# Kernel optimization log

Measured on AMD Instinct MI355X. Metric: run time of the kernel, lower is better.

The kernel has to match this reference:

```python
import jax, jax.numpy as jnp
import numpy as np

BS, V, S, K = 4, 2048, 7, 10
CLASS_NUM, VEC_NUM, CAT = 6, 8, 16
OUT_HEAD = CLASS_NUM + VEC_NUM * 3  # 30
DIM_FUSE = 128 + 128 + 256 + 256 + 512 + 512 + 16  # 1808


def _normalize(x, axis):
    return x / jnp.maximum(jnp.linalg.norm(x, axis=axis, keepdims=True), 1e-12)


def knn_index(verts, k):
    # verts: (b, v, 3) -> (b, v, k) excluding self
    inner = jnp.einsum('bnd,bmd->bnm', verts, verts)
    sq = jnp.sum(verts * verts, axis=2)
    dist = sq[:, :, None] + sq[:, None, :] - 2.0 * inner
    _, idx = jax.lax.top_k(-dist, k + 1)
    return idx[:, :, 1:]


def nearest_index(target, source):
    # target: (b, v1, 3), source: (b, v2, 3) -> (b, v1)
    inner = jnp.einsum('bnd,bmd->bnm', target, source)
    d = jnp.sum(source * source, 2)[:, None, :] + jnp.sum(target * target, 2)[:, :, None] - 2.0 * inner
    return jnp.argmin(d, axis=-1)


def gather_nb(t, idx):
    # t: (b, v, d), idx: (b, v1, k) -> (b, v1, k, d)
    return jax.vmap(lambda tt, ii: tt[ii])(t, idx)


def gather1(t, idx):
    # t: (b, v, d), idx: (b, v1) -> (b, v1, d)
    return jax.vmap(lambda tt, ii: tt[ii])(t, idx)


def bn_train(x, g, b, eps=1e-5):
    # x: (b, v, c); BatchNorm1d training-mode over (batch, vertices)
    m = jnp.mean(x, axis=(0, 1), keepdims=True)
    v = jnp.var(x, axis=(0, 1), keepdims=True)
    return (x - m) * jax.lax.rsqrt(v + eps) * g + b


def conv_surface(nb_idx, verts, directions, s, kernel_num):
    nd = _normalize(gather_nb(verts, nb_idx) - verts[:, :, None, :], -1)  # (b,v,n,3)
    sd = _normalize(directions, 0)  # (3, s*k)
    theta = jax.nn.relu(jnp.einsum('bvnd,dk->bvnk', nd, sd))
    b_, v_, n_, _ = theta.shape
    theta = theta.reshape(b_, v_, n_, s, kernel_num)
    return jnp.sum(jnp.max(theta, axis=2), axis=2)  # (b, v, kernel_num)


def conv_layer(nb_idx, verts, fm, w, b, directions, s, out_ch):
    nd = _normalize(gather_nb(verts, nb_idx) - verts[:, :, None, :], -1)
    sd = _normalize(directions, 0)  # (3, s*out_ch)
    theta = jax.nn.relu(jnp.einsum('bvnd,dk->bvnk', nd, sd))  # (b,v,n,s*o)
    fo = jnp.einsum('bvc,ck->bvk', fm, w) + b  # (b, v, (s+1)*o)
    center = fo[..., :out_ch]
    supp = gather_nb(fo[..., out_ch:], nb_idx)  # (b,v,n,s*o)
    act = (theta * supp).reshape(theta.shape[0], theta.shape[1], theta.shape[2], s, out_ch)
    act = jnp.sum(jnp.max(act, axis=2), axis=2)  # (b, v, o)
    return center + act


def pool_layer(verts, fm, pooling_rate, nb_num):
    idx = knn_index(verts, nb_num)
    pooled = jnp.max(gather_nb(fm, idx), axis=2)
    pool_num = verts.shape[1] // pooling_rate
    # deterministic subsample (torch uses randperm; fixed arange for reproducibility)
    return verts[:, :pool_num], pooled[:, :pool_num]


def setup_inputs() -> dict:
    key = jax.random.key(0)
    ks = jax.random.split(key, 16)
    def rn(i, shape, scale=0.05):
        return jax.random.normal(ks[i], shape, dtype=jnp.float32) * scale
    z = lambda *s: jnp.zeros(s, jnp.float32)
    o = lambda *s: jnp.ones(s, jnp.float32)
    return {
        'vertices': jax.random.normal(ks[0], (BS, V, 3), dtype=jnp.float32),
        'onehot': jax.nn.one_hot(jax.random.randint(ks[1], (BS,), 0, CAT), CAT, dtype=jnp.float32),
        'dir0': rn(2, (3, S * 128)),
        'w1': rn(3, (128, (S + 1) * 128)), 'b1': z((S + 1) * 128), 'dir1': rn(4, (3, S * 128)),
        'w2': rn(5, (128, (S + 1) * 256)), 'b2': z((S + 1) * 256), 'dir2': rn(6, (3, S * 256)),
        'w3': rn(7, (256, (S + 1) * 256)), 'b3': z((S + 1) * 256), 'dir3': rn(8, (3, S * 256)),
        'w4': rn(9, (256, (S + 1) * 512)), 'b4': z((S + 1) * 512), 'dir4': rn(10, (3, S * 512)),
        'g_bn1': o(128), 'be_bn1': z(128),
        'g_bn2': o(256), 'be_bn2': z(256),
        'g_bn3': o(256), 'be_bn3': z(256),
        'wc1': rn(11, (512, DIM_FUSE)), 'bc1': z(512),
        'wc2': rn(12, (512, 512)), 'bc2': z(512),
        'wc3': rn(13, (OUT_HEAD, 512)), 'bc3': z(OUT_HEAD),
    }


def reference(vertices, onehot, dir0, w1, b1, dir1, w2, b2, dir2, w3, b3, dir3,
              w4, b4, dir4, g_bn1, be_bn1, g_bn2, be_bn2, g_bn3, be_bn3,
              wc1, bc1, wc2, bc2, wc3, bc3):
    bs, v_num, _ = vertices.shape
    nb = knn_index(vertices, K)
    fm0 = jax.nn.relu(conv_surface(nb, vertices, dir0, S, 128))
    fm1 = jax.nn.relu(bn_train(conv_layer(nb, vertices, fm0, w1, b1, dir1, S, 128), g_bn1, be_bn1))
    vp1, fp1 = pool_layer(vertices, fm1, 4, 4)
    nb1 = knn_index(vp1, min(K, vp1.shape[1] // 8))
    fm2 = jax.nn.relu(bn_train(conv_layer(nb1, vp1, fp1, w2, b2, dir2, S, 256), g_bn2, be_bn2))
    fm3 = jax.nn.relu(bn_train(conv_layer(nb1, vp1, fm2, w3, b3, dir3, S, 256), g_bn3, be_bn3))
    vp2, fp2 = pool_layer(vp1, fm3, 4, 4)
    nb2 = knn_index(vp2, min(K, vp2.shape[1] // 8))
    fm4 = conv_layer(nb2, vp2, fp2, w4, b4, dir4, S, 512)
    f_global = jnp.max(fm4, axis=1)  # (b, 512)
    n1 = nearest_index(vertices, vp1)
    n2 = nearest_index(vertices, vp2)
    fm2u = gather1(fm2, n1)
    fm3u = gather1(fm3, n1)
    fm4u = gather1(fm4, n2)
    fg = jnp.broadcast_to(f_global[:, None, :], (bs, v_num, 512))
    oh = jnp.broadcast_to(onehot[:, None, :], (bs, v_num, CAT))
    feat = jnp.concatenate([fm0, fm1, fm2u, fm3u, fm4u, oh], axis=2)
    fuse = jnp.concatenate([fm0, fm1, fm2u, fm3u, fm4u, fg, oh], axis=2)
    h = jax.nn.relu(jnp.einsum('bvc,oc->bvo', fuse, wc1) + bc1)
    h = jax.nn.relu(jnp.einsum('bvc,oc->bvo', h, wc2) + bc2)
    pred = jnp.einsum('bvc,oc->bvo', h, wc3) + bc3
    seg = pred[..., :CLASS_NUM]
    vecs = pred[..., CLASS_NUM:CLASS_NUM + VEC_NUM * 3]
    return (seg, vecs, feat)
```

## Files before the change

### kernel.cpp

```cpp
#include <hip/hip_runtime.h>
#include <hip/hip_bf16.h>
#include <math.h>

#define BSZ 4
#define VN 2048
#define SS 7
#define KNB 10

typedef __attribute__((ext_vector_type(8))) short short8;
typedef __attribute__((ext_vector_type(4))) float f32x4;

__device__ inline ushort f2bf(float x) {
    __hip_bfloat16 h = __float2bfloat16(x);
    return *(ushort*)&h;
}

__device__ inline unsigned fenc(float f) {
    unsigned b = __float_as_uint(f);
    return (b & 0x80000000u) ? ~b : (b | 0x80000000u);
}
__device__ inline float fdec(unsigned e) {
    unsigned b = (e & 0x80000000u) ? (e & 0x7FFFFFFFu) : ~e;
    return __uint_as_float(b);
}

#define PB0 8960L
#define PB1 24320L
#define PB2 958208L
#define PB3 1220352L
#define PB4 3186432L

__global__ void prep_uber(const float* __restrict__ d0, const float* __restrict__ d1,
                          const float* __restrict__ d2, const float* __restrict__ d3,
                          const float* __restrict__ d4,
                          float* __restrict__ s0, float* __restrict__ s1,
                          float* __restrict__ s2, float* __restrict__ s3, float* __restrict__ s4,
                          const float* __restrict__ wc3, float* __restrict__ wc3t,
                          const float* __restrict__ wc1, ushort* __restrict__ wc1b,
                          const float* __restrict__ wc2, ushort* __restrict__ wc2b,
                          const float* __restrict__ w1, const float* __restrict__ w2,
                          const float* __restrict__ w3, const float* __restrict__ w4,
                          ushort* __restrict__ o1, ushort* __restrict__ o2,
                          ushort* __restrict__ o3, ushort* __restrict__ o4) {
    long i = blockIdx.x * 256L + threadIdx.x;
    if (i < PB0) {
        const float* src; float* dst; int C, c;
        if (i < 896)        { src = d0; dst = s0; C = 896;  c = (int)i; }
        else if (i < 1792)  { src = d1; dst = s1; C = 896;  c = (int)i - 896; }
        else if (i < 3584)  { src = d2; dst = s2; C = 1792; c = (int)i - 1792; }
        else if (i < 5376)  { src = d3; dst = s3; C = 1792; c = (int)i - 3584; }
        else                { src = d4; dst = s4; C = 3584; c = (int)i - 5376; }
        float a = src[c], b = src[C + c], e = src[2 * C + c];
        float den = fmaxf(sqrtf(a * a + b * b + e * e), 1e-12f);
        dst[c] = a / den; dst[C + c] = b / den; dst[2 * C + c] = e / den;
    } else if (i < PB1) {
        long j = i - PB0;
        int o = (int)(j / 512), k = (int)(j % 512);
        wc3t[(long)k * 30 + o] = wc3[j];
    } else if (i < PB2) {
        long j = i - PB1;
        int c = (int)(j % 1824);
        long r = j / 1824;
        wc1b[j] = f2bf(c < 1808 ? wc1[r * 1808 + c] : 0.f);
    } else if (i < PB3) {
        long j = i - PB2;
        wc2b[j] = f2bf(wc2[j]);
    } else if (i < PB4) {
        long j = i - PB3;
        const float* w; ushort* o; int K, N;
        if (j < 131072)       { w = w1; o = o1; K = 128; N = 1024; }
        else if (j < 393216)  { w = w2; o = o2; K = 128; N = 2048; j -= 131072; }
        else if (j < 917504)  { w = w3; o = o3; K = 256; N = 2048; j -= 393216; }
        else                  { w = w4; o = o4; K = 256; N = 4096; j -= 917504; }
        int n = (int)(j / K), k = (int)(j % K);
        o[j] = f2bf(w[(long)k * N + n]);
    }
}

#define KOFF0 0L
#define KOFF1 1310720L
#define KOFF2 1392640L
#define KOFF3 1397760L
#define KOFF4 1528832L
#define KTOT  1537024L

template <int KK>
__device__ void knn_part_dev(const float* __restrict__ verts, int Nsrc, int T, int nch,
                             int tile, int b, int ch,
                             float* __restrict__ pd, int* __restrict__ pi,
                             float* sx, float* sy, float* sz) {
    int len = Nsrc / nch;
    const float* vb = verts + (long)b * VN * 3;
    int j0 = ch * len;
    for (int j = threadIdx.x; j < len; j += 256) {
        sx[j] = vb[(j0 + j) * 3 + 0];
        sy[j] = vb[(j0 + j) * 3 + 1];
        sz[j] = vb[(j0 + j) * 3 + 2];
    }
    __syncthreads();
    int i = tile * 256 + threadIdx.x;
    if (i >= T) return;
    float px = vb[i * 3], py = vb[i * 3 + 1], pz = vb[i * 3 + 2];
    float d[KK]; int id[KK];
#pragma unroll
    for (int q = 0; q < KK; q++) { d[q] = 1e30f; id[q] = 0; }
    for (int j = 0; j < len; j++) {
        float dx = sx[j] - px, dy = sy[j] - py, dz = sz[j] - pz;
        float dd = dx * dx + dy * dy + dz * dz;
        int jj = j0 + j;
        dd = (jj == i) ? 1e30f : dd;
        if (__any(dd < d[KK - 1])) {
#pragma unroll
            for (int q = 0; q < KK; q++) {
                bool lt = dd < d[q];
                float dmin = lt ? dd : d[q];
                float dmax = lt ? d[q] : dd;
                int imin = lt ? jj : id[q];
                int imax = lt ? id[q] : jj;
                d[q] = dmin; id[q] = imin; dd = dmax; jj = imax;
            }
        }
    }
    long base = (((long)b * T + i) * nch + ch) * KK;
#pragma unroll
    for (int q = 0; q < KK; q++) { pd[base + q] = d[q]; pi[base + q] = id[q]; }
}

__device__ void nearest_dev(const float* __restrict__ verts, int SN, int* __restrict__ out,
                            int gl, float* sx, float* sy, float* sz) {
    int t = gl * 256 + threadIdx.x;
    int b = t / VN;
    const float* vb = verts + (long)b * VN * 3;
    for (int j = threadIdx.x; j < SN; j += 256) {
        sx[j] = vb[j * 3]; sy[j] = vb[j * 3 + 1]; sz[j] = vb[j * 3 + 2];
    }
    __syncthreads();
    int i = t % VN;
    float px = vb[i * 3], py = vb[i * 3 + 1], pz = vb[i * 3 + 2];
    float best = 1e30f; int bi = 0;
    for (int j = 0; j < SN; j++) {
        float dx = sx[j] - px, dy = sy[j] - py, dz = sz[j] - pz;
        float dd = dx * dx + dy * dy + dz * dz;
        bool lt = dd < best;
        best = lt ? dd : best;
        bi = lt ? j : bi;
    }
    out[t] = bi;
}

__global__ __launch_bounds__(256) void knn_part_uber(const float* __restrict__ verts,
                                                     float* __restrict__ pd, int* __restrict__ pi,
                                                     int* __restrict__ n1, int* __restrict__ n2) {
    __shared__ float smem[3 * 512];
    int gb = blockIdx.x;
    if (gb < 512) {
        int tile = gb % 8, bc = gb / 8;
        knn_part_dev<10>(verts, 2048, 2048, 16, tile, bc / 16, bc % 16, pd + KOFF0, pi + KOFF0,
                         smem, smem + 128, smem + 256);
    } else if (gb < 544) {
        int local = gb - 512, tile = local % 2, bc = local / 2;
        knn_part_dev<10>(verts, 512, 512, 4, tile, bc / 4, bc % 4, pd + KOFF1, pi + KOFF1,
                         smem, smem + 128, smem + 256);
    } else if (gb < 548) {
        int bc = gb - 544;
        knn_part_dev<10>(verts, 128, 128, 1, 0, bc, 0, pd + KOFF2, pi + KOFF2,
                         smem, smem + 128, smem + 256);
    } else if (gb < 676) {
        int local = gb - 548, tile = local % 2, bc = local / 2;
        knn_part_dev<4>(verts, 2048, 512, 16, tile, bc / 16, bc % 16, pd + KOFF3, pi + KOFF3,
                        smem, smem + 128, smem + 256);
    } else if (gb < 692) {
        int bc = gb - 676;
        knn_part_dev<4>(verts, 512, 128, 4, 0, bc / 4, bc % 4, pd + KOFF4, pi + KOFF4,
                        smem, smem + 128, smem + 256);
    } else if (gb < 724) {
        nearest_dev(verts, 512, n1, gb - 692, smem, smem + 512, smem + 1024);
    } else {
        nearest_dev(verts, 128, n2, gb - 724, smem, smem + 512, smem + 1024);
    }
}

template <int KK, int NCH>
__device__ void knn_merge_dev(const float* __restrict__ pd, const int* __restrict__ pi,
                              int t, int* __restrict__ out) {
    float d[KK]; int id[KK];
#pragma unroll
    for (int q = 0; q < KK; q++) { d[q] = 1e30f; id[q] = 0; }
    for (int c = 0; c < NCH; c++) {
        long base = ((long)t * NCH + c) * KK;
        for (int q = 0; q < KK; q++) {
            float dd = pd[base + q];
            if (dd >= d[KK - 1]) break;
            int jj = pi[base + q];
#pragma unroll
            for (int p = 0; p < KK; p++) {
                bool lt = dd < d[p];
                float dmin = lt ? dd : d[p];
                float dmax = lt ? d[p] : dd;
                int imin = lt ? jj : id[p];
                int imax = lt ? id[p] : jj;
                d[p] = dmin; id[p] = imin; dd = dmax; jj = imax;
            }
        }
    }
#pragma unroll
    for (int q = 0; q < KK; q++) out[(long)t * KK + q] = id[q];
}

__global__ void knn_merge_uber(const float* __restrict__ pd, const int* __restrict__ pi,
                               int* __restrict__ nb, int* __restrict__ nb1, int* __restrict__ nb2,
                               int* __restrict__ nbp1, int* __restrict__ nbp2) {
    int gt = blockIdx.x * 256 + threadIdx.x;
    if (gt < 8192)       knn_merge_dev<10, 16>(pd + KOFF0, pi + KOFF0, gt, nb);
    else if (gt < 10240) knn_merge_dev<10, 4>(pd + KOFF1, pi + KOFF1, gt - 8192, nb1);
    else if (gt < 10752) knn_merge_dev<10, 1>(pd + KOFF2, pi + KOFF2, gt - 10240, nb2);
    else if (gt < 12800) knn_merge_dev<4, 16>(pd + KOFF3, pi + KOFF3, gt - 10752, nbp1);
    else                 knn_merge_dev<4, 4>(pd + KOFF4, pi + KOFF4, gt - 12800, nbp2);
}

__global__ void conv_surface_kernel(const float* __restrict__ verts, const int* __restrict__ nb,
                                    const float* __restrict__ sd, float* __restrict__ fm0,
                                    ushort* __restrict__ fm0b) {
    int bv = blockIdx.x;
    int b = bv / VN, v = bv % VN;
    __shared__ float snd[KNB][3];
    int tid = threadIdx.x;
    if (tid < KNB) {
        int nj = nb[(long)bv * KNB + tid];
        const float* vb = verts + (long)b * VN * 3;
        float dx = vb[nj * 3] - vb[v * 3];
        float dy = vb[nj * 3 + 1] - vb[v * 3 + 1];
        float dz = vb[nj * 3 + 2] - vb[v * 3 + 2];
        float den = fmaxf(sqrtf(dx * dx + dy * dy + dz * dz), 1e-12f);
        snd[tid][0] = dx / den; snd[tid][1] = dy / den; snd[tid][2] = dz / den;
    }
    __syncthreads();
    int c = tid;
    float acc = 0.f;
    for (int s = 0; s < SS; s++) {
        int col = s * 128 + c;
        float s0 = sd[col], s1 = sd[896 + col], s2 = sd[2 * 896 + col];
        float m = 0.f;
#pragma unroll
        for (int n = 0; n < KNB; n++) {
            float dot = snd[n][0] * s0 + snd[n][1] * s1 + snd[n][2] * s2;
            m = fmaxf(m, dot);
        }
        acc += m;
    }
    fm0[(long)bv * 128 + c] = acc;
    fm0b[(long)bv * 128 + c] = f2bf(acc);
}

__global__ void conv_act_kernel(const float* __restrict__ verts, const int* __restrict__ nb,
                                const float* __restrict__ sd, const float* __restrict__ fo,
                                float* __restrict__ out, unsigned* __restrict__ fgmax,
                                int Vl, int outC) {
    int bv = blockIdx.x;
    int b = bv / Vl, v = bv % Vl;
    __shared__ float snd[KNB][3];
    __shared__ int srow[KNB];
    int tid = threadIdx.x;
    if (tid < KNB) {
        int nj = nb[(long)bv * KNB + tid];
        srow[tid] = b * Vl + nj;
        const float* vb = verts + (long)b * VN * 3;
        float dx = vb[nj * 3] - vb[v * 3];
        float dy = vb[nj * 3 + 1] - vb[v * 3 + 1];
        float dz = vb[nj * 3 + 2] - vb[v * 3 + 2];
        float den = fmaxf(sqrtf(dx * dx + dy * dy + dz * dz), 1e-12f);
        snd[tid][0] = dx / den; snd[tid][1] = dy / den; snd[tid][2] = dz / den;
    }
    __syncthreads();
    int c = tid;
    int SC = SS * outC;
    int foN = SC + outC;
    float acc = fo[(long)bv * foN + c];
    for (int s = 0; s < SS; s++) {
        int col = s * outC + c;
        float s0 = sd[col], s1 = sd[SC + col], s2 = sd[2 * SC + col];
        float m = -1e30f;
#pragma unroll
        for (int n = 0; n < KNB; n++) {
            float dot = snd[n][0] * s0 + snd[n][1] * s1 + snd[n][2] * s2;
            float th = fmaxf(dot, 0.f);
            float sup = fo[(long)srow[n] * foN + outC + col];
            m = fmaxf(m, th * sup);
        }
        acc += m;
    }
    out[(long)bv * outC + c] = acc;
    if (fgmax) atomicMax(&fgmax[b * outC + c], fenc(acc));
}

__global__ __launch_bounds__(256) void bn_stat_kernel(const float* __restrict__ x,
                                                      float* __restrict__ stat, int R, int C) {
    int rp = 256 / C;
    int c = threadIdx.x % C;
    int rs = threadIdx.x / C;
    float s = 0.f, s2 = 0.f;
    for (long r = (long)blockIdx.x * rp + rs; r < R; r += (long)gridDim.x * rp) {
        float v = x[r * C + c];
        s += v; s2 += v * v;
    }
    atomicAdd(&stat[c], s);
    atomicAdd(&stat[C + c], s2);
}

__global__ void bn_apply_relu_kernel(const float* __restrict__ x, const float* __restrict__ stat,
                                     const float* __restrict__ g, const float* __restrict__ be,
                                     float* __restrict__ out, ushort* __restrict__ outb, int R, int C) {
    long i = blockIdx.x * 256L + threadIdx.x;
    if (i >= (long)R * C) return;
    int c = (int)(i % C);
    float mu = stat[c] / R;
    float var = stat[C + c] / R - mu * mu;
    var = fmaxf(var, 0.f);
    float y = (x[i] - mu) * rsqrtf(var + 1e-5f) * g[c] + be[c];
    y = fmaxf(y, 0.f);
    out[i] = y;
    if (outb) outb[i] = f2bf(y);
}

__global__ void pool_b_kernel(const float* __restrict__ fm, const int* __restrict__ idx,
                              ushort* __restrict__ out, int Vin, int T, int C) {
    long i = blockIdx.x * 256L + threadIdx.x;
    if (i >= (long)BSZ * T * C) return;
    int c = (int)(i % C);
    long bt = i / C;
    int b = (int)(bt / T), t = (int)(bt % T);
    const int* id = idx + ((long)b * T + t) * 4;
    float m = -1e30f;
#pragma unroll
    for (int n = 0; n < 4; n++)
        m = fmaxf(m, fm[((long)b * Vin + id[n]) * C + c]);
    out[i] = f2bf(m);
}

__global__ __launch_bounds__(256) void gemm_mfma_bt_kernel(
    const ushort* __restrict__ A, const ushort* __restrict__ Bt,
    const float* __restrict__ bias, float* __restrict__ Cf, ushort* __restrict__ Cb,
    int M, int N, int K, int relu)
{
    __shared__ ushort As[128 * 32];
    __shared__ ushort Bs[128 * 32];
    int t = threadIdx.x;
    int w = t >> 6, l = t & 63;
    int quad = l >> 4, lm = l & 15;
    int wm = w >> 1, wn = w & 1;
    long m0 = blockIdx.y * 128L;
    long n0 = blockIdx.x * 128L;
    int lr = t >> 2;
    int lk = (t & 3) * 8;
    f32x4 acc[4][4];
#pragma unroll
    for (int i = 0; i < 4; i++)
#pragma unroll
        for (int j = 0; j < 4; j++) acc[i][j] = (f32x4){0.f, 0.f, 0.f, 0.f};

    for (int k0 = 0; k0 < K; k0 += 32) {
        uint4 a0 = *(const uint4*)(A + (m0 + lr) * K + k0 + lk);
        uint4 a1 = *(const uint4*)(A + (m0 + 64 + lr) * K + k0 + lk);
        uint4 b0 = *(const uint4*)(Bt + (n0 + lr) * K + k0 + lk);
        uint4 b1 = *(const uint4*)(Bt + (n0 + 64 + lr) * K + k0 + lk);
        __syncthreads();
        *(uint4*)&As[lr * 32 + lk] = a0;
        *(uint4*)&As[(64 + lr) * 32 + lk] = a1;
        *(uint4*)&Bs[lr * 32 + lk] = b0;
        *(uint4*)&Bs[(64 + lr) * 32 + lk] = b1;
        __syncthreads();
        short8 af[4], bfr[4];
#pragma unroll
        for (int i = 0; i < 4; i++)
            af[i] = *(const short8*)&As[(wm * 64 + i * 16 + lm) * 32 + quad * 8];
#pragma unroll
        for (int j = 0; j < 4; j++)
            bfr[j] = *(const short8*)&Bs[(wn * 64 + j * 16 + lm) * 32 + quad * 8];
#pragma unroll
        for (int i = 0; i < 4; i++)
#pragma unroll
            for (int j = 0; j < 4; j++)
                acc[i][j] = __builtin_amdgcn_mfma_f32_16x16x32_bf16(af[i], bfr[j], acc[i][j], 0, 0, 0);
    }
#pragma unroll
    for (int i = 0; i < 4; i++) {
#pragma unroll
        for (int j = 0; j < 4; j++) {
            int n = (int)n0 + wn * 64 + j * 16 + lm;
            float bv = bias[n];
#pragma unroll
            for (int r = 0; r < 4; r++) {
                int m = (int)m0 + wm * 64 + i * 16 + quad * 4 + r;
                float v = acc[i][j][r] + bv;
                if (relu) v = fmaxf(v, 0.f);
                if (Cf) Cf[(long)m * N + n] = v;
                if (Cb) Cb[(long)m * N + n] = f2bf(v);
            }
        }
    }
}

__global__ __launch_bounds__(256) void gemm_mfma_bt64_kernel(
    const ushort* __restrict__ A, const ushort* __restrict__ Bt,
    const float* __restrict__ bias, float* __restrict__ Cf, ushort* __restrict__ Cb,
    int M, int N, int K, int relu)
{
    __shared__ ushort As[64 * 32];
    __shared__ ushort Bs[128 * 32];
    int t = threadIdx.x;
    int w = t >> 6, l = t & 63;
    int quad = l >> 4, lm = l & 15;
    int wm = w >> 1, wn = w & 1;
    long m0 = blockIdx.y * 64L;
    long n0 = blockIdx.x * 128L;
    int lr = t >> 2;
    int lk = (t & 3) * 8;
    f32x4 acc[2][4];
#pragma unroll
    for (int i = 0; i < 2; i++)
#pragma unroll
        for (int j = 0; j < 4; j++) acc[i][j] = (f32x4){0.f, 0.f, 0.f, 0.f};

    for (int k0 = 0; k0 < K; k0 += 32) {
        uint4 a0 = *(const uint4*)(A + (m0 + lr) * K + k0 + lk);
        uint4 b0 = *(const uint4*)(Bt + (n0 + lr) * K + k0 + lk);
        uint4 b1 = *(const uint4*)(Bt + (n0 + 64 + lr) * K + k0 + lk);
        __syncthreads();
        *(uint4*)&As[lr * 32 + lk] = a0;
        *(uint4*)&Bs[lr * 32 + lk] = b0;
        *(uint4*)&Bs[(64 + lr) * 32 + lk] = b1;
        __syncthreads();
        short8 af[2], bfr[4];
#pragma unroll
        for (int i = 0; i < 2; i++)
            af[i] = *(const short8*)&As[(wm * 32 + i * 16 + lm) * 32 + quad * 8];
#pragma unroll
        for (int j = 0; j < 4; j++)
            bfr[j] = *(const short8*)&Bs[(wn * 64 + j * 16 + lm) * 32 + quad * 8];
#pragma unroll
        for (int i = 0; i < 2; i++)
#pragma unroll
            for (int j = 0; j < 4; j++)
                acc[i][j] = __builtin_amdgcn_mfma_f32_16x16x32_bf16(af[i], bfr[j], acc[i][j], 0, 0, 0);
    }
#pragma unroll
    for (int i = 0; i < 2; i++) {
#pragma unroll
        for (int j = 0; j < 4; j++) {
            int n = (int)n0 + wn * 64 + j * 16 + lm;
            float bv = bias[n];
#pragma unroll
            for (int r = 0; r < 4; r++) {
                int m = (int)m0 + wm * 32 + i * 16 + quad * 4 + r;
                float v = acc[i][j][r] + bv;
                if (relu) v = fmaxf(v, 0.f);
                if (Cf) Cf[(long)m * N + n] = v;
                if (Cb) Cb[(long)m * N + n] = f2bf(v);
            }
        }
    }
}

__global__ __launch_bounds__(256) void wc3_kernel(const float* __restrict__ h2,
                                                  const float* __restrict__ wc3t,
                                                  const float* __restrict__ bc3,
                                                  float* __restrict__ out) {
    int r8 = threadIdx.x >> 5;
    int c = threadIdx.x & 31;
    long row = blockIdx.x * 8L + r8;
    const float* hr = h2 + row * 512;
    float acc = 0.f;
    if (c < 30) {
        for (int k = 0; k < 512; k++)
            acc += hr[k] * wc3t[k * 30 + c];
        acc += bc3[c];
        if (c < 6) out[row * 6 + c] = acc;
        else       out[49152 + row * 24 + (c - 6)] = acc;
    }
}

__global__ void fuse_bf_kernel(const float* __restrict__ fm0, const float* __restrict__ fm1,
                               const float* __restrict__ fm2, const float* __restrict__ fm3,
                               const float* __restrict__ fm4, const unsigned* __restrict__ fg_enc,
                               const float* __restrict__ onehot,
                               const int* __restrict__ n1, const int* __restrict__ n2,
                               ushort* __restrict__ fuse_b, float* __restrict__ feat) {
    long i = blockIdx.x * 256L + threadIdx.x;
    if (i >= 8192L * 1824) return;
    int c = (int)(i % 1824);
    long row = i / 1824;
    int b = (int)(row / VN);
    float val = 0.f;
    if (c < 128)       val = fm0[row * 128 + c];
    else if (c < 256)  val = fm1[row * 128 + (c - 128)];
    else if (c < 512)  val = fm2[((long)b * 512 + n1[row]) * 256 + (c - 256)];
    else if (c < 768)  val = fm3[((long)b * 512 + n1[row]) * 256 + (c - 512)];
    else if (c < 1280) val = fm4[((long)b * 128 + n2[row]) * 512 + (c - 768)];
    else if (c < 1792) val = fdec(fg_enc[b * 512 + (c - 1280)]);
    else if (c < 1808) val = onehot[b * 16 + (c - 1792)];
    fuse_b[i] = f2bf(val);
    if (c < 1280)                   feat[row * 1296 + c] = val;
    else if (c >= 1792 && c < 1808) feat[row * 1296 + (c - 512)] = val;
}


extern "C" void kernel_launch(void* const* d_in, const int* in_sizes, int n_in,
                              void* d_out, int out_size, void* d_ws, size_t ws_size,
                              hipStream_t stream) {
    const float* verts  = (const float*)d_in[0];
    const float* onehot = (const float*)d_in[1];
    const float* dir0 = (const float*)d_in[2];
    const float* w1 = (const float*)d_in[3];
    const float* b1 = (const float*)d_in[4];
    const float* dir1 = (const float*)d_in[5];
    const float* w2 = (const float*)d_in[6];
    const float* b2 = (const float*)d_in[7];
    const float* dir2 = (const float*)d_in[8];
    const float* w3 = (const float*)d_in[9];
    const float* b3 = (const float*)d_in[10];
    const float* dir3 = (const float*)d_in[11];
    const float* w4 = (const float*)d_in[12];
    const float* b4 = (const float*)d_in[13];
    const float* dir4 = (const float*)d_in[14];
    const float* g_bn1 = (const float*)d_in[15];
    const float* be_bn1 = (const float*)d_in[16];
    const float* g_bn2 = (const float*)d_in[17];
    const float* be_bn2 = (const float*)d_in[18];
    const float* g_bn3 = (const float*)d_in[19];
    const float* be_bn3 = (const float*)d_in[20];
    const float* wc1 = (const float*)d_in[21];
    const float* bc1 = (const float*)d_in[22];
    const float* wc2 = (const float*)d_in[23];
    const float* bc2 = (const float*)d_in[24];
    const float* wc3 = (const float*)d_in[25];
    const float* bc3 = (const float*)d_in[26];
    float* outf = (float*)d_out;

    float* wsf = (float*)d_ws;
    size_t off = 0;
    auto alloc = [&](size_t n) { float* p = wsf + off; off += (n + 15) & ~(size_t)15; return p; };

    float* sd0 = alloc(3 * 896);
    float* sd1 = alloc(3 * 896);
    float* sd2 = alloc(3 * 1792);
    float* sd3 = alloc(3 * 1792);
    float* sd4 = alloc(3 * 3584);
    float* wc3t = alloc(512L * 30);
    float* fm0 = alloc(8192L * 128);
    float* fm1 = alloc(8192L * 128);
    float* c1  = alloc(8192L * 128);
    float* fm2 = alloc(2048L * 256);
    float* c2  = alloc(2048L * 256);
    float* fm3 = alloc(2048L * 256);
    float* c3  = alloc(2048L * 256);
    float* fm4 = alloc(512L * 512);
    float* statbase = alloc(3328);
    float* stat1 = statbase;
    float* stat2 = statbase + 256;
    float* stat3 = statbase + 768;
    unsigned* fg_enc = (unsigned*)(statbase + 1280);
    float* fbuf = alloc(8192L * 1024);
    float* h2 = alloc(8192L * 512);
    float* pd  = alloc(KTOT);
    int* pi    = (int*)alloc(KTOT);
    int* nb   = (int*)alloc(8192L * KNB);
    int* nb1  = (int*)alloc(2048L * KNB);
    int* nb2  = (int*)alloc(512L * KNB);
    int* nbp1 = (int*)alloc(2048L * 4);
    int* nbp2 = (int*)alloc(512L * 4);
    int* n1   = (int*)alloc(8192);
    int* n2   = (int*)alloc(8192);
    ushort* fuse_b = (ushort*)alloc(8192L * 1824 / 2);
    ushort* h1b    = (ushort*)alloc(8192L * 512 / 2);
    ushort* wc1b   = (ushort*)alloc(512L * 1824 / 2);
    ushort* wc2b   = (ushort*)alloc(512L * 512 / 2);
    ushort* w1tb   = (ushort*)alloc(1024L * 128 / 2);
    ushort* w2tb   = (ushort*)alloc(2048L * 128 / 2);
    ushort* w3tb   = (ushort*)alloc(2048L * 256 / 2);
    ushort* w4tb   = (ushort*)alloc(4096L * 256 / 2);
    ushort* fm0b   = (ushort*)alloc(8192L * 128 / 2);
    ushort* fp1b   = (ushort*)alloc(2048L * 128 / 2);
    ushort* fm2b   = (ushort*)alloc(2048L * 256 / 2);
    ushort* fp2b   = (ushort*)alloc(512L * 256 / 2);

    auto nblk = [](long n, int b) { return (unsigned)((n + b - 1) / b); };

    hipMemsetAsync(statbase, 0, 3328 * sizeof(float), stream);
    prep_uber<<<nblk(PB4, 256), 256, 0, stream>>>(dir0, dir1, dir2, dir3, dir4,
                                                  sd0, sd1, sd2, sd3, sd4,
                                                  wc3, wc3t, wc1, wc1b, wc2, wc2b,
                                                  w1, w2, w3, w4, w1tb, w2tb, w3tb, w4tb);

    knn_part_uber<<<756, 256, 0, stream>>>(verts, pd, pi, n1, n2);
    knn_merge_uber<<<52, 256, 0, stream>>>(pd, pi, nb, nb1, nb2, nbp1, nbp2);

    conv_surface_kernel<<<BSZ * 2048, 128, 0, stream>>>(verts, nb, sd0, fm0, fm0b);

    gemm_mfma_bt_kernel<<<dim3(8, 64), 256, 0, stream>>>(fm0b, w1tb, b1, fbuf, nullptr, 8192, 1024, 128, 0);
    conv_act_kernel<<<BSZ * 2048, 128, 0, stream>>>(verts, nb, sd1, fbuf, c1, nullptr, 2048, 128);
    bn_stat_kernel<<<256, 256, 0, stream>>>(c1, stat1, 8192, 128);
    bn_apply_relu_kernel<<<nblk(8192L * 128, 256), 256, 0, stream>>>(c1, stat1, g_bn1, be_bn1, fm1, nullptr, 8192, 128);

    pool_b_kernel<<<nblk(BSZ * 512L * 128, 256), 256, 0, stream>>>(fm1, nbp1, fp1b, 2048, 512, 128);

    gemm_mfma_bt64_kernel<<<dim3(16, 32), 256, 0, stream>>>(fp1b, w2tb, b2, fbuf, nullptr, 2048, 2048, 128, 0);
    conv_act_kernel<<<BSZ * 512, 256, 0, stream>>>(verts, nb1, sd2, fbuf, c2, nullptr, 512, 256);
    bn_stat_kernel<<<256, 256, 0, stream>>>(c2, stat2, 2048, 256);
    bn_apply_relu_kernel<<<nblk(2048L * 256, 256), 256, 0, stream>>>(c2, stat2, g_bn2, be_bn2, fm2, fm2b, 2048, 256);

    gemm_mfma_bt64_kernel<<<dim3(16, 32), 256, 0, stream>>>(fm2b, w3tb, b3, fbuf, nullptr, 2048, 2048, 256, 0);
    conv_act_kernel<<<BSZ * 512, 256, 0, stream>>>(verts, nb1, sd3, fbuf, c3, nullptr, 512, 256);
    bn_stat_kernel<<<256, 256, 0, stream>>>(c3, stat3, 2048, 256);
    bn_apply_relu_kernel<<<nblk(2048L * 256, 256), 256, 0, stream>>>(c3, stat3, g_bn3, be_bn3, fm3, nullptr, 2048, 256);

    pool_b_kernel<<<nblk(BSZ * 128L * 256, 256), 256, 0, stream>>>(fm3, nbp2, fp2b, 512, 128, 256);

    gemm_mfma_bt64_kernel<<<dim3(32, 8), 256, 0, stream>>>(fp2b, w4tb, b4, fbuf, nullptr, 512, 4096, 256, 0);
    conv_act_kernel<<<BSZ * 128, 512, 0, stream>>>(verts, nb2, sd4, fbuf, fm4, fg_enc, 128, 512);

    fuse_bf_kernel<<<nblk(8192L * 1824, 256), 256, 0, stream>>>(fm0, fm1, fm2, fm3, fm4, fg_enc, onehot,
                                                                n1, n2, fuse_b, outf + 245760);

    gemm_mfma_bt64_kernel<<<dim3(4, 128), 256, 0, stream>>>(fuse_b, wc1b, bc1, nullptr, h1b, 8192, 512, 1824, 1);
    gemm_mfma_bt64_kernel<<<dim3(4, 128), 256, 0, stream>>>(h1b, wc2b, bc2, h2, nullptr, 8192, 512, 512, 1);
    wc3_kernel<<<1024, 256, 0, stream>>>(h2, wc3t, bc3, outf);
}
```

Before: 515.8 us.

## Tile weight transposes through shared memory and use dot-product form in kNN

Moves the bf16 transpose of the four conv weight matrices out of the flat prep kernel into a dedicated 32x32 shared-memory tiled transpose kernel, so both the global reads and the writes are coalesced. The kNN and nearest-neighbour searches now stage each source point in shared memory as a float4 holding xyz and its squared norm. Distance is computed as |s|^2 - 2 p·s, which drops the per-point |p|^2 constant and leaves the ordering unchanged. This saves arithmetic and uses one vector LDS load per point, but adds a kernel launch and may change near-tie ordering through rounding.

```diff
diff --git a/kernel.cpp b/kernel.cpp
--- a/kernel.cpp
+++ b/kernel.cpp
@@ -28,7 +28,6 @@
 #define PB1 24320L
 #define PB2 958208L
 #define PB3 1220352L
-#define PB4 3186432L
 
 __global__ void prep_uber(const float* __restrict__ d0, const float* __restrict__ d1,
                           const float* __restrict__ d2, const float* __restrict__ d3,
@@ -37,11 +36,7 @@
                           float* __restrict__ s2, float* __restrict__ s3, float* __restrict__ s4,
                           const float* __restrict__ wc3, float* __restrict__ wc3t,
                           const float* __restrict__ wc1, ushort* __restrict__ wc1b,
-                          const float* __restrict__ wc2, ushort* __restrict__ wc2b,
-                          const float* __restrict__ w1, const float* __restrict__ w2,
-                          const float* __restrict__ w3, const float* __restrict__ w4,
-                          ushort* __restrict__ o1, ushort* __restrict__ o2,
-                          ushort* __restrict__ o3, ushort* __restrict__ o4) {
+                          const float* __restrict__ wc2, ushort* __restrict__ wc2b) {
     long i = blockIdx.x * 256L + threadIdx.x;
     if (i < PB0) {
         const float* src; float* dst; int C, c;
@@ -65,16 +60,30 @@
     } else if (i < PB3) {
         long j = i - PB2;
         wc2b[j] = f2bf(wc2[j]);
-    } else if (i < PB4) {
-        long j = i - PB3;
-        const float* w; ushort* o; int K, N;
-        if (j < 131072)       { w = w1; o = o1; K = 128; N = 1024; }
-        else if (j < 393216)  { w = w2; o = o2; K = 128; N = 2048; j -= 131072; }
-        else if (j < 917504)  { w = w3; o = o3; K = 256; N = 2048; j -= 393216; }
-        else                  { w = w4; o = o4; K = 256; N = 4096; j -= 917504; }
-        int n = (int)(j / K), k = (int)(j % K);
-        o[j] = f2bf(w[(long)k * N + n]);
-    }
+    }
+}
+
+__global__ __launch_bounds__(256) void wt_trans_all(const float* __restrict__ w1, const float* __restrict__ w2,
+                                                    const float* __restrict__ w3, const float* __restrict__ w4,
+                                                    ushort* __restrict__ o1, ushort* __restrict__ o2,
+                                                    ushort* __restrict__ o3, ushort* __restrict__ o4) {
+    __shared__ float tile[32][33];
+    int gb = blockIdx.x;
+    const float* w; ushort* o; int K, N, t;
+    if (gb < 128)      { w = w1; o = o1; K = 128; N = 1024; t = gb; }
+    else if (gb < 384) { w = w2; o = o2; K = 128; N = 2048; t = gb - 128; }
+    else if (gb < 896) { w = w3; o = o3; K = 256; N = 2048; t = gb - 384; }
+    else               { w = w4; o = o4; K = 256; N = 4096; t = gb - 896; }
+    int tn = t % (N / 32), tk = t / (N / 32);
+    int n0 = tn * 32, k0 = tk * 32;
+    int tx = threadIdx.x % 32, ty = threadIdx.x / 32;
+#pragma unroll
+    for (int r = 0; r < 32; r += 8)
+        tile[ty + r][tx] = w[(long)(k0 + ty + r) * N + n0 + tx];
+    __syncthreads();
+#pragma unroll
+    for (int r = 0; r < 32; r += 8)
+        o[(long)(n0 + ty + r) * K + k0 + tx] = f2bf(tile[tx][ty + r]);
 }
 
 #define KOFF0 0L
@@ -88,14 +97,15 @@
 __device__ void knn_part_dev(const float* __restrict__ verts, int Nsrc, int T, int nch,
                              int tile, int b, int ch,
                              float* __restrict__ pd, int* __restrict__ pi,
-                             float* sx, float* sy, float* sz) {
+                             float4* __restrict__ s4) {
     int len = Nsrc / nch;
     const float* vb = verts + (long)b * VN * 3;
     int j0 = ch * len;
     for (int j = threadIdx.x; j < len; j += 256) {
-        sx[j] = vb[(j0 + j) * 3 + 0];
-        sy[j] = vb[(j0 + j) * 3 + 1];
-        sz[j] = vb[(j0 + j) * 3 + 2];
+        float x = vb[(j0 + j) * 3 + 0];
+        float y = vb[(j0 + j) * 3 + 1];
+        float z = vb[(j0 + j) * 3 + 2];
+        s4[j] = make_float4(x, y, z, x * x + y * y + z * z);
     }
     __syncthreads();
     int i = tile * 256 + threadIdx.x;
@@ -105,8 +115,9 @@
 #pragma unroll
     for (int q = 0; q < KK; q++) { d[q] = 1e30f; id[q] = 0; }
     for (int j = 0; j < len; j++) {
-        float dx = sx[j] - px, dy = sy[j] - py, dz = sz[j] - pz;
-        float dd = dx * dx + dy * dy + dz * dz;
+        float4 s = s4[j];
+        float dot = px * s.x + py * s.y + pz * s.z;
+        float dd = fmaf(-2.f, dot, s.w);
         int jj = j0 + j;
         dd = (jj == i) ? 1e30f : dd;
         if (__any(dd < d[KK - 1])) {
@@ -127,20 +138,22 @@
 }
 
 __device__ void nearest_dev(const float* __restrict__ verts, int SN, int* __restrict__ out,
-                            int gl, float* sx, float* sy, float* sz) {
+                            int gl, float4* __restrict__ s4) {
     int t = gl * 256 + threadIdx.x;
     int b = t / VN;
     const float* vb = verts + (long)b * VN * 3;
     for (int j = threadIdx.x; j < SN; j += 256) {
-        sx[j] = vb[j * 3]; sy[j] = vb[j * 3 + 1]; sz[j] = vb[j * 3 + 2];
+        float x = vb[j * 3], y = vb[j * 3 + 1], z = vb[j * 3 + 2];
+        s4[j] = make_float4(x, y, z, x * x + y * y + z * z);
     }
     __syncthreads();
     int i = t % VN;
     float px = vb[i * 3], py = vb[i * 3 + 1], pz = vb[i * 3 + 2];
     float best = 1e30f; int bi = 0;
     for (int j = 0; j < SN; j++) {
-        float dx = sx[j] - px, dy = sy[j] - py, dz = sz[j] - pz;
-        float dd = dx * dx + dy * dy + dz * dz;
+        float4 s = s4[j];
+        float dot = px * s.x + py * s.y + pz * s.z;
+        float dd = fmaf(-2.f, dot, s.w);
         bool lt = dd < best;
         best = lt ? dd : best;
         bi = lt ? j : bi;
@@ -151,32 +164,27 @@
 __global__ __launch_bounds__(256) void knn_part_uber(const float* __restrict__ verts,
                                                      float* __restrict__ pd, int* __restrict__ pi,
                                                      int* __restrict__ n1, int* __restrict__ n2) {
-    __shared__ float smem[3 * 512];
+    __shared__ float4 smem[512];
     int gb = blockIdx.x;
     if (gb < 512) {
         int tile = gb % 8, bc = gb / 8;
-        knn_part_dev<10>(verts, 2048, 2048, 16, tile, bc / 16, bc % 16, pd + KOFF0, pi + KOFF0,
-                         smem, smem + 128, smem + 256);
+        knn_part_dev<10>(verts, 2048, 2048, 16, tile, bc / 16, bc % 16, pd + KOFF0, pi + KOFF0, smem);
     } else if (gb < 544) {
         int local = gb - 512, tile = local % 2, bc = local / 2;
-        knn_part_dev<10>(verts, 512, 512, 4, tile, bc / 4, bc % 4, pd + KOFF1, pi + KOFF1,
-                         smem, smem + 128, smem + 256);
+        knn_part_dev<10>(verts, 512, 512, 4, tile, bc / 4, bc % 4, pd + KOFF1, pi + KOFF1, smem);
     } else if (gb < 548) {
         int bc = gb - 544;
-        knn_part_dev<10>(verts, 128, 128, 1, 0, bc, 0, pd + KOFF2, pi + KOFF2,
-                         smem, smem + 128, smem + 256);
+        knn_part_dev<10>(verts, 128, 128, 1, 0, bc, 0, pd + KOFF2, pi + KOFF2, smem);
     } else if (gb < 676) {
         int local = gb - 548, tile = local % 2, bc = local / 2;
-        knn_part_dev<4>(verts, 2048, 512, 16, tile, bc / 16, bc % 16, pd + KOFF3, pi + KOFF3,
-                        smem, smem + 128, smem + 256);
+        knn_part_dev<4>(verts, 2048, 512, 16, tile, bc / 16, bc % 16, pd + KOFF3, pi + KOFF3, smem);
     } else if (gb < 692) {
         int bc = gb - 676;
-        knn_part_dev<4>(verts, 512, 128, 4, 0, bc / 4, bc % 4, pd + KOFF4, pi + KOFF4,
-                        smem, smem + 128, smem + 256);
+        knn_part_dev<4>(verts, 512, 128, 4, 0, bc / 4, bc % 4, pd + KOFF4, pi + KOFF4, smem);
     } else if (gb < 724) {
-        nearest_dev(verts, 512, n1, gb - 692, smem, smem + 512, smem + 1024);
+        nearest_dev(verts, 512, n1, gb - 692, smem);
     } else {
-        nearest_dev(verts, 128, n2, gb - 724, smem, smem + 512, smem + 1024);
+        nearest_dev(verts, 128, n2, gb - 724, smem);
     }
 }
 
@@ -586,10 +594,10 @@
     auto nblk = [](long n, int b) { return (unsigned)((n + b - 1) / b); };
 
     hipMemsetAsync(statbase, 0, 3328 * sizeof(float), stream);
-    prep_uber<<<nblk(PB4, 256), 256, 0, stream>>>(dir0, dir1, dir2, dir3, dir4,
+    prep_uber<<<nblk(PB3, 256), 256, 0, stream>>>(dir0, dir1, dir2, dir3, dir4,
                                                   sd0, sd1, sd2, sd3, sd4,
-                                                  wc3, wc3t, wc1, wc1b, wc2, wc2b,
-                                                  w1, w2, w3, w4, w1tb, w2tb, w3tb, w4tb);
+                                                  wc3, wc3t, wc1, wc1b, wc2, wc2b);
+    wt_trans_all<<<1920, 256, 0, stream>>>(w1, w2, w3, w4, w1tb, w2tb, w3tb, w4tb);
 
     knn_part_uber<<<756, 256, 0, stream>>>(verts, pd, pi, n1, n2);
     knn_merge_uber<<<52, 256, 0, stream>>>(pd, pi, nb, nb1, nb2, nbp1, nbp2);
```

Result: faster. 505.1 us (-2.1%).
